# Kernel tuning notes

Measured on AMD Instinct MI355X. Metric: run time of the kernel, lower is better.

The kernel has to match this reference:

```python
import jax, jax.numpy as jnp
import numpy as np

B, LC, LQ, D = 64, 1024, 128, 128
NEG_BIG = 1.0e12


def _len_mask(seq_len, T):
    # seq_len: (B,1) int. Equivalent to 1 - cumsum(one_hot(L, T)): 1 for pos < L.
    pos = jnp.arange(T)  # (T,)
    return (pos[None, :] < seq_len).astype(jnp.float32)  # (B,T)


def setup_inputs() -> dict:
    key = jax.random.key(0)
    ks = jax.random.split(key, 7)
    return {
        "x_cont": jax.random.normal(ks[0], (B, LC, D), dtype=jnp.float32),
        "x_ques": jax.random.normal(ks[1], (B, LQ, D), dtype=jnp.float32),
        "W0": jax.random.normal(ks[2], (D, 1), dtype=jnp.float32) / np.sqrt(D),
        "W1": jax.random.normal(ks[3], (D, 1), dtype=jnp.float32) / np.sqrt(D),
        "W2": jax.random.normal(ks[4], (1, 1, D), dtype=jnp.float32) / np.sqrt(D),
        "cont_len": jax.random.randint(ks[5], (B, 1), 1, LC, dtype=jnp.int32),
        "ques_len": jax.random.randint(ks[6], (B, 1), 1, LQ, dtype=jnp.int32),
    }


def reference(x_cont, x_ques, W0, W1, W2, cont_len, ques_len):
    # Trilinear similarity: S[b,c,q] = x_cont@W0 + x_ques@W1 + (x_cont*W2) . x_ques
    s_cont = jnp.einsum('bcd,do->bco', x_cont, W0)            # (B,LC,1)
    s_ques = jnp.einsum('bqd,do->boq', x_ques, W1)            # (B,1,LQ)
    s_fuse = jnp.einsum('bcd,bqd->bcq', x_cont * W2, x_ques)  # (B,LC,LQ)
    S = s_cont + s_ques + s_fuse                               # (B,LC,LQ)

    mask_q = _len_mask(ques_len, LQ)  # (B,LQ)
    mask_c = _len_mask(cont_len, LC)  # (B,LC)

    # Softmax over query axis, masking invalid query positions (axis=-1)
    S_bar = jax.nn.softmax(S - (1.0 - mask_q)[:, None, :] * NEG_BIG, axis=-1)
    # Softmax over context axis, masking invalid context positions, then transpose
    S_T = jnp.swapaxes(
        jax.nn.softmax(S - (1.0 - mask_c)[:, :, None] * NEG_BIG, axis=1), 1, 2
    )  # (B,LQ,LC)

    c2q = jnp.einsum('bcq,bqd->bcd', S_bar, x_ques)             # (B,LC,D)
    q2c = jnp.einsum('bcq,bqk,bkd->bcd', S_bar, S_T, x_cont)    # (B,LC,D)

    result = jnp.concatenate(
        [x_cont, c2q, x_cont * c2q, x_cont * q2c], axis=-1
    )  # (B,LC,4D)
    return result, S_bar, S_T
```

## Files before the change

kernel.cpp:

```cpp
#include <hip/hip_runtime.h>

#define NB 64
#define LC 1024
#define LQ 128
#define DD 128
#define NEG_BIG 1.0e12f

typedef __attribute__((ext_vector_type(8))) short short8;
typedef __attribute__((ext_vector_type(4))) unsigned short ushort4v;
typedef __attribute__((ext_vector_type(4))) float floatx4;

__device__ __forceinline__ float wave_reduce_max(float v) {
#pragma unroll
  for (int m = 32; m >= 1; m >>= 1) v = fmaxf(v, __shfl_xor(v, m, 64));
  return v;
}
__device__ __forceinline__ float wave_reduce_sum(float v) {
#pragma unroll
  for (int m = 32; m >= 1; m >>= 1) v += __shfl_xor(v, m, 64);
  return v;
}
__device__ __forceinline__ unsigned short f2bf(float f) {
  union { float f; unsigned int u; } v;
  v.f = f;
  const unsigned int r = v.u + 0x7FFFu + ((v.u >> 16) & 1u);
  return (unsigned short)(r >> 16);
}
__device__ __forceinline__ float bf2f(unsigned int u) {
  union { unsigned int u; float f; } v;
  v.u = u << 16;
  return v.f;
}

__global__ __launch_bounds__(256) void k_pre_c(
    const float* __restrict__ xc, const float* __restrict__ W0,
    unsigned short* __restrict__ xcb, unsigned short* __restrict__ xcT,
    float* __restrict__ a_cont) {
  __shared__ __align__(16) unsigned short tile[64 * 136];
  const int b = blockIdx.x >> 4;
  const int c0 = (blockIdx.x & 15) << 6;
  const int t = threadIdx.x;
  const int w = t >> 6, lane = t & 63;
  const float* src = xc + ((size_t)b * LC + c0) * DD;
  unsigned short* dstb = xcb + ((size_t)b * LC + c0) * DD;

#pragma unroll
  for (int i = 0; i < 8; ++i) {
    const int id = t + (i << 8);
    const int row = id >> 5, u = id & 31;
    const float4 v = *(const float4*)(src + (size_t)row * DD + (u << 2));
    ushort4v pk;
    pk[0] = f2bf(v.x); pk[1] = f2bf(v.y); pk[2] = f2bf(v.z); pk[3] = f2bf(v.w);
    *(ushort4v*)(tile + row * 136 + (u << 2)) = pk;
    *(ushort4v*)(dstb + (size_t)row * DD + (u << 2)) = pk;
  }
  const float w0a = W0[lane << 1];
  const float w0b = W0[(lane << 1) + 1];
  __syncthreads();
#pragma unroll
  for (int r = 0; r < 16; ++r) {
    const int row = (w << 4) + r;
    const unsigned int pk = *(const unsigned int*)(tile + row * 136 + (lane << 1));
    float s = fmaf(bf2f(pk & 0xffffu), w0a, bf2f(pk >> 16) * w0b);
    s = wave_reduce_sum(s);
    if (lane == 0) a_cont[b * LC + c0 + row] = s;
  }
  const int d = t >> 1, ch = t & 1;
  short8 o[4];
#pragma unroll
  for (int j = 0; j < 32; ++j)
    ((unsigned short*)o)[j] = tile[(ch * 32 + j) * 136 + d];
  unsigned short* dp = xcT + ((size_t)b * DD + d) * LC + c0 + ch * 32;
#pragma unroll
  for (int j = 0; j < 4; ++j) *(short8*)(dp + (j << 3)) = o[j];
}

__global__ __launch_bounds__(256) void k_pre_q(
    const float* __restrict__ xq, const float* __restrict__ W1,
    const float* __restrict__ W2, unsigned short* __restrict__ xqwb,
    unsigned short* __restrict__ xqT, float* __restrict__ a_ques) {
  __shared__ __align__(16) unsigned short tile[128 * 136];
  const int b = blockIdx.x;
  const int t = threadIdx.x;
  const int w = t >> 6, lane = t & 63;
  const float* src = xq + (size_t)b * LQ * DD;
  unsigned short* dstw = xqwb + (size_t)b * LQ * DD;

#pragma unroll
  for (int i = 0; i < 16; ++i) {
    const int id = t + (i << 8);
    const int row = id >> 5, u = id & 31;
    const float4 v = *(const float4*)(src + (size_t)row * DD + (u << 2));
    const float4 wv = *(const float4*)(W2 + (u << 2));
    ushort4v pk, pf;
    pk[0] = f2bf(v.x); pk[1] = f2bf(v.y); pk[2] = f2bf(v.z); pk[3] = f2bf(v.w);
    pf[0] = f2bf(v.x * wv.x); pf[1] = f2bf(v.y * wv.y);
    pf[2] = f2bf(v.z * wv.z); pf[3] = f2bf(v.w * wv.w);
    *(ushort4v*)(tile + row * 136 + (u << 2)) = pk;
    *(ushort4v*)(dstw + (size_t)row * DD + (u << 2)) = pf;
  }
  const float w1a = W1[lane << 1];
  const float w1b = W1[(lane << 1) + 1];
  __syncthreads();
#pragma unroll
  for (int r = 0; r < 32; ++r) {
    const int row = (w << 5) + r;
    const unsigned int pk = *(const unsigned int*)(tile + row * 136 + (lane << 1));
    float s = fmaf(bf2f(pk & 0xffffu), w1a, bf2f(pk >> 16) * w1b);
    s = wave_reduce_sum(s);
    if (lane == 0) a_ques[b * LQ + row] = s;
  }
  const int d = t >> 1, ch = t & 1;
  short8 o[8];
#pragma unroll
  for (int j = 0; j < 64; ++j)
    ((unsigned short*)o)[j] = tile[(ch * 64 + j) * 136 + d];
  unsigned short* dp = xqT + ((size_t)b * DD + d) * LQ + ch * 64;
#pragma unroll
  for (int j = 0; j < 8; ++j) *(short8*)(dp + (j << 3)) = o[j];
}

#define PADW 136

__global__ __launch_bounds__(512) void k_score(
    const unsigned short* __restrict__ xcb, const unsigned short* __restrict__ xqwb,
    const float* __restrict__ a_cont, const float* __restrict__ a_ques,
    const int* __restrict__ qlen_p, float* __restrict__ out_sbar,
    float* __restrict__ out_st) {
  __shared__ __align__(16) unsigned short smem[2 * 128 * PADW];
  unsigned short* xcs = smem;
  unsigned short* xqs = smem + 128 * PADW;
  float* s_tile = (float*)smem;

  const int b = blockIdx.x >> 3;
  const int c0 = (blockIdx.x & 7) << 7;
  const int t = threadIdx.x;
  const int w = t >> 6, lane = t & 63;
  const int frow = lane & 15;
  const int kb = lane >> 4;

  const unsigned short* xcb_blk = xcb + ((size_t)b * LC + c0) * DD;
  const unsigned short* xqw_b = xqwb + (size_t)b * LQ * DD;

#pragma unroll
  for (int i = 0; i < 4; ++i) {
    const int id = t + (i << 9);
    const int row = id >> 4, u = id & 15;
    *(short8*)(xcs + row * PADW + (u << 3)) =
        *(const short8*)(xcb_blk + (size_t)row * DD + (u << 3));
    *(short8*)(xqs + row * PADW + (u << 3)) =
        *(const short8*)(xqw_b + (size_t)row * DD + (u << 3));
  }

  const int qlen = qlen_p[b];
  float ac[4], aq[8];
#pragma unroll
  for (int reg = 0; reg < 4; ++reg)
    ac[reg] = a_cont[b * LC + c0 + w * 16 + kb * 4 + reg];
#pragma unroll
  for (int n = 0; n < 8; ++n) aq[n] = a_ques[b * LQ + n * 16 + frow];

  __syncthreads();

  floatx4 acc[8];
#pragma unroll
  for (int n = 0; n < 8; ++n) acc[n] = (floatx4){0.f, 0.f, 0.f, 0.f};
  const unsigned short* arow = xcs + (w * 16 + frow) * PADW + kb * 8;
  const unsigned short* brow = xqs + frow * PADW + kb * 8;
#pragma unroll
  for (int ks = 0; ks < 4; ++ks) {
    const short8 af = *(const short8*)(arow + ks * 32);
#pragma unroll
    for (int n = 0; n < 8; ++n) {
      const short8 bf = *(const short8*)(brow + n * 16 * PADW + ks * 32);
      acc[n] = __builtin_amdgcn_mfma_f32_16x16x32_bf16(af, bf, acc[n], 0, 0, 0);
    }
  }

  float raw[8][4];
#pragma unroll
  for (int n = 0; n < 8; ++n)
#pragma unroll
    for (int reg = 0; reg < 4; ++reg) raw[n][reg] = acc[n][reg] + ac[reg] + aq[n];

  float* sbar_row0 =
      out_sbar + ((size_t)b * LC + c0 + w * 16 + kb * 4) * LQ + frow;
#pragma unroll
  for (int reg = 0; reg < 4; ++reg) {
    float x[8];
    float m = -3.4e38f;
#pragma unroll
    for (int n = 0; n < 8; ++n) {
      x[n] = raw[n][reg] - ((n * 16 + frow) < qlen ? 0.f : NEG_BIG);
      m = fmaxf(m, x[n]);
    }
#pragma unroll
    for (int msk = 8; msk >= 1; msk >>= 1) m = fmaxf(m, __shfl_xor(m, msk, 64));
    float s = 0.f;
#pragma unroll
    for (int n = 0; n < 8; ++n) {
      x[n] = __expf(x[n] - m);
      s += x[n];
    }
#pragma unroll
    for (int msk = 8; msk >= 1; msk >>= 1) s += __shfl_xor(s, msk, 64);
    const float inv = 1.0f / s;
    float* o = sbar_row0 + (size_t)reg * LQ;
#pragma unroll
    for (int n = 0; n < 8; ++n) o[n * 16] = x[n] * inv;
  }

  float* st_b = out_st + (size_t)b * LQ * LC;
#pragma unroll
  for (int p = 0; p < 4; ++p) {
    __syncthreads();
#pragma unroll
    for (int n2 = 0; n2 < 2; ++n2) {
#pragma unroll
      for (int reg = 0; reg < 4; ++reg)
        s_tile[(n2 * 16 + frow) * 132 + (w * 16 + kb * 4 + reg)] =
            raw[2 * p + n2][reg];
    }
    __syncthreads();
    const int qrow = t >> 4;
    const int cch = t & 15;
    const float4 u0 = *(const float4*)(s_tile + qrow * 132 + (cch << 2));
    const float4 u1 = *(const float4*)(s_tile + qrow * 132 + ((cch + 16) << 2));
    float* dst = st_b + (size_t)(p * 32 + qrow) * LC + c0;
    *(float4*)(dst + (cch << 2)) = u0;
    *(float4*)(dst + ((cch + 16) << 2)) = u1;
  }
}

#define PSTR 1028

__global__ __launch_bounds__(256) void k_fuse(
    float* __restrict__ st, const unsigned short* __restrict__ xcT,
    const int* __restrict__ clen_p, unsigned short* __restrict__ AbT) {
  __shared__ __align__(16) unsigned short P[16 * PSTR];
  __shared__ __align__(16) unsigned short bt[128 * 72];
  __shared__ unsigned short abt[128 * 20];
  __shared__ float inv_s[16];

  const int b = blockIdx.x >> 3;
  const int q0 = (blockIdx.x & 7) << 4;
  const int t = threadIdx.x;
  const int w = t >> 6, lane = t & 63;
  const int frow = lane & 15, kb = lane >> 4;
  const int L = clen_p[b];
  float* st_blk = st + ((size_t)b * LQ + q0) * LC;

#pragma unroll
  for (int r = 0; r < 4; ++r) {
    const int row = (w << 2) + r;
    float* rowp = st_blk + (size_t)row * LC;
    float4 v[4];
    float m = -3.4e38f;
#pragma unroll
    for (int ph = 0; ph < 4; ++ph) {
      const int c = (lane << 2) + (ph << 8);
      v[ph] = *(const float4*)(rowp + c);
      if (c + 0 < L) m = fmaxf(m, v[ph].x);
      if (c + 1 < L) m = fmaxf(m, v[ph].y);
      if (c + 2 < L) m = fmaxf(m, v[ph].z);
      if (c + 3 < L) m = fmaxf(m, v[ph].w);
    }
    m = wave_reduce_max(m);
    float s = 0.f;
#pragma unroll
    for (int ph = 0; ph < 4; ++ph) {
      const int c = (lane << 2) + (ph << 8);
      v[ph].x = (c + 0 < L) ? __expf(v[ph].x - m) : 0.f;
      v[ph].y = (c + 1 < L) ? __expf(v[ph].y - m) : 0.f;
      v[ph].z = (c + 2 < L) ? __expf(v[ph].z - m) : 0.f;
      v[ph].w = (c + 3 < L) ? __expf(v[ph].w - m) : 0.f;
      s += (v[ph].x + v[ph].y) + (v[ph].z + v[ph].w);
      ushort4v pk;
      pk[0] = f2bf(v[ph].x); pk[1] = f2bf(v[ph].y);
      pk[2] = f2bf(v[ph].z); pk[3] = f2bf(v[ph].w);
      *(ushort4v*)(P + row * PSTR + c) = pk;
    }
    s = wave_reduce_sum(s);
    const float inv = 1.0f / s;
    if (lane == 0) inv_s[row] = inv;
#pragma unroll
    for (int ph = 0; ph < 4; ++ph) {
      const int c = (lane << 2) + (ph << 8);
      *(float4*)(rowp + c) =
          make_float4(v[ph].x * inv, v[ph].y * inv, v[ph].z * inv, v[ph].w * inv);
    }
  }

  const unsigned short* xcT_b = xcT + (size_t)b * DD * LC;
  floatx4 acc0 = (floatx4){0.f, 0.f, 0.f, 0.f};
  floatx4 acc1 = (floatx4){0.f, 0.f, 0.f, 0.f};
  for (int kc = 0; kc < 16; ++kc) {
    __syncthreads();
#pragma unroll
    for (int i = 0; i < 4; ++i) {
      const int id = t + (i << 8);
      const int row = id >> 3, u = id & 7;
      *(short8*)(bt + row * 72 + (u << 3)) =
          *(const short8*)(xcT_b + (size_t)row * LC + (kc << 6) + (u << 3));
    }
    __syncthreads();
#pragma unroll
    for (int ks = 0; ks < 2; ++ks) {
      const short8 af =
          *(const short8*)(P + frow * PSTR + (kc << 6) + ks * 32 + kb * 8);
      const short8 b0 =
          *(const short8*)(bt + ((w * 2 + 0) * 16 + frow) * 72 + ks * 32 + kb * 8);
      const short8 b1 =
          *(const short8*)(bt + ((w * 2 + 1) * 16 + frow) * 72 + ks * 32 + kb * 8);
      acc0 = __builtin_amdgcn_mfma_f32_16x16x32_bf16(af, b0, acc0, 0, 0, 0);
      acc1 = __builtin_amdgcn_mfma_f32_16x16x32_bf16(af, b1, acc1, 0, 0, 0);
    }
  }
  __syncthreads();
  const float i0 = inv_s[kb * 4 + 0], i1 = inv_s[kb * 4 + 1];
  const float i2 = inv_s[kb * 4 + 2], i3 = inv_s[kb * 4 + 3];
  {
    const int d0 = (w * 2 + 0) * 16 + frow;
    abt[d0 * 20 + kb * 4 + 0] = f2bf(acc0[0] * i0);
    abt[d0 * 20 + kb * 4 + 1] = f2bf(acc0[1] * i1);
    abt[d0 * 20 + kb * 4 + 2] = f2bf(acc0[2] * i2);
    abt[d0 * 20 + kb * 4 + 3] = f2bf(acc0[3] * i3);
    const int d1 = (w * 2 + 1) * 16 + frow;
    abt[d1 * 20 + kb * 4 + 0] = f2bf(acc1[0] * i0);
    abt[d1 * 20 + kb * 4 + 1] = f2bf(acc1[1] * i1);
    abt[d1 * 20 + kb * 4 + 2] = f2bf(acc1[2] * i2);
    abt[d1 * 20 + kb * 4 + 3] = f2bf(acc1[3] * i3);
  }
  __syncthreads();
  const int d = t >> 1, h = t & 1;
  short8 ov;
#pragma unroll
  for (int j = 0; j < 8; ++j)
    ((unsigned short*)&ov)[j] = abt[d * 20 + h * 8 + j];
  *(short8*)(AbT + ((size_t)b * DD + d) * LQ + q0 + h * 8) = ov;
}

__global__ __launch_bounds__(256) void k_out(
    const float* __restrict__ xc, const float* __restrict__ sbar,
    const unsigned short* __restrict__ xqT, const unsigned short* __restrict__ AbT,
    float* __restrict__ out) {
  __shared__ __align__(16) float stg[2 * 32 * 132];
  unsigned short* sbs = (unsigned short*)stg;

  const int b = blockIdx.x >> 4;
  const int c0 = (blockIdx.x & 15) << 6;
  const int t = threadIdx.x;
  const int w = t >> 6, lane = t & 63;
  const int frow = lane & 15, kb = lane >> 4;

  const float* sb_blk = sbar + ((size_t)b * LC + c0) * LQ;
#pragma unroll
  for (int i = 0; i < 8; ++i) {
    const int id = t + (i << 8);
    const int row = id >> 5, u = id & 31;
    const float4 v = *(const float4*)(sb_blk + (size_t)row * LQ + (u << 2));
    ushort4v pk;
    pk[0] = f2bf(v.x); pk[1] = f2bf(v.y); pk[2] = f2bf(v.z); pk[3] = f2bf(v.w);
    *(ushort4v*)(sbs + row * 136 + (u << 2)) = pk;
  }

  const unsigned short* xqT_b = xqT + (size_t)b * DD * LQ;
  const unsigned short* AbT_b = AbT + (size_t)b * DD * LQ;
  short8 bq[2][4], ba[2][4];
#pragma unroll
  for (int nt = 0; nt < 2; ++nt) {
    const int d = (w << 5) + (nt << 4) + frow;
#pragma unroll
    for (int ks = 0; ks < 4; ++ks) {
      bq[nt][ks] = *(const short8*)(xqT_b + (size_t)d * LQ + ks * 32 + kb * 8);
      ba[nt][ks] = *(const short8*)(AbT_b + (size_t)d * LQ + ks * 32 + kb * 8);
    }
  }
  __syncthreads();

  floatx4 accq[4][2], acca[4][2];
#pragma unroll
  for (int mt = 0; mt < 4; ++mt)
#pragma unroll
    for (int nt = 0; nt < 2; ++nt) {
      accq[mt][nt] = (floatx4){0.f, 0.f, 0.f, 0.f};
      acca[mt][nt] = (floatx4){0.f, 0.f, 0.f, 0.f};
    }
#pragma unroll
  for (int mt = 0; mt < 4; ++mt) {
#pragma unroll
    for (int ks = 0; ks < 4; ++ks) {
      const short8 af =
          *(const short8*)(sbs + ((mt << 4) + frow) * 136 + ks * 32 + kb * 8);
#pragma unroll
      for (int nt = 0; nt < 2; ++nt) {
        accq[mt][nt] =
            __builtin_amdgcn_mfma_f32_16x16x32_bf16(af, bq[nt][ks], accq[mt][nt], 0, 0, 0);
        acca[mt][nt] =
            __builtin_amdgcn_mfma_f32_16x16x32_bf16(af, ba[nt][ks], acca[mt][nt], 0, 0, 0);
      }
    }
  }

  float* out_b = out + ((size_t)b * LC + c0) * (4 * DD);
  const float* xc_blk = xc + ((size_t)b * LC + c0) * DD;

#pragma unroll
  for (int p = 0; p < 2; ++p) {
    __syncthreads();
#pragma unroll
    for (int mh = 0; mh < 2; ++mh) {
      const int mt = 2 * p + mh;
#pragma unroll
      for (int nt = 0; nt < 2; ++nt) {
        const int d = (w << 5) + (nt << 4) + frow;
        const int cl = (mh << 4) + (kb << 2);
#pragma unroll
        for (int reg = 0; reg < 4; ++reg) {
          stg[(cl + reg) * 132 + d] = accq[mt][nt][reg];
          stg[32 * 132 + (cl + reg) * 132 + d] = acca[mt][nt][reg];
        }
      }
    }
    __syncthreads();
    const int g = lane >> 4;
    const int d0 = (lane & 15) << 3;
#pragma unroll
    for (int j = 0; j < 8; ++j) {
      const int rl = (w << 3) + j;
      const int c = (p << 5) + rl;
      const float4 xv0 = *(const float4*)(xc_blk + (size_t)c * DD + d0);
      const float4 xv1 = *(const float4*)(xc_blk + (size_t)c * DD + d0 + 4);
      const float4 cq0 = *(const float4*)(stg + rl * 132 + d0);
      const float4 cq1 = *(const float4*)(stg + rl * 132 + d0 + 4);
      const float4 qc0 = *(const float4*)(stg + 32 * 132 + rl * 132 + d0);
      const float4 qc1 = *(const float4*)(stg + 32 * 132 + rl * 132 + d0 + 4);
      float4 o0, o1;
      if (g == 0) { o0 = xv0; o1 = xv1; }
      else if (g == 1) { o0 = cq0; o1 = cq1; }
      else if (g == 2) {
        o0 = make_float4(xv0.x * cq0.x, xv0.y * cq0.y, xv0.z * cq0.z, xv0.w * cq0.w);
        o1 = make_float4(xv1.x * cq1.x, xv1.y * cq1.y, xv1.z * cq1.z, xv1.w * cq1.w);
      } else {
        o0 = make_float4(xv0.x * qc0.x, xv0.y * qc0.y, xv0.z * qc0.z, xv0.w * qc0.w);
        o1 = make_float4(xv1.x * qc1.x, xv1.y * qc1.y, xv1.z * qc1.z, xv1.w * qc1.w);
      }
      float* o = out_b + (size_t)c * (4 * DD) + (g << 7) + d0;
      *(float4*)(o) = o0;
      *(float4*)(o + 4) = o1;
    }
  }
}

extern "C" void kernel_launch(void* const* d_in, const int* in_sizes, int n_in,
                              void* d_out, int out_size, void* d_ws, size_t ws_size,
                              hipStream_t stream) {
  const float* xc = (const float*)d_in[0];
  const float* xq = (const float*)d_in[1];
  const float* W0 = (const float*)d_in[2];
  const float* W1 = (const float*)d_in[3];
  const float* W2 = (const float*)d_in[4];
  const int* clen = (const int*)d_in[5];
  const int* qlen = (const int*)d_in[6];

  float* out = (float*)d_out;
  float* out_sbar = out + (size_t)NB * LC * 4 * DD;
  float* out_st = out_sbar + (size_t)NB * LC * LQ;

  float* a_cont = (float*)d_ws;
  float* a_ques = a_cont + NB * LC;
  unsigned short* xcb = (unsigned short*)(a_ques + NB * LQ);
  unsigned short* xcT = xcb + (size_t)NB * LC * DD;
  unsigned short* xqwb = xcT + (size_t)NB * LC * DD;
  unsigned short* xqT = xqwb + (size_t)NB * LQ * DD;
  unsigned short* AbT = xqT + (size_t)NB * LQ * DD;

  k_pre_c<<<NB * 16, 256, 0, stream>>>(xc, W0, xcb, xcT, a_cont);
  k_pre_q<<<NB, 256, 0, stream>>>(xq, W1, W2, xqwb, xqT, a_ques);
  k_score<<<NB * 8, 512, 0, stream>>>(xcb, xqwb, a_cont, a_ques, qlen,
                                      out_sbar, out_st);
  k_fuse<<<NB * 8, 256, 0, stream>>>(out_st, xcT, clen, AbT);
  k_out<<<NB * 16, 256, 0, stream>>>(xc, out_sbar, xqT, AbT, out);
}
```

Before: 123.1 us.

## Pass unnormalized bf16 column exponentials and partial sums from score to fuse kernel

The score kernel now applies the context-length mask and exponentiates the scores itself. It writes them as bf16 along with per-tile column partial sums, replacing the fp32 S_T round trip in which the fuse kernel re-read, normalized and rewrote every score. The fuse kernel only rescales the bf16 values and reuses them as the MFMA operand. The bf16 copies of x_cont and x_ques*W2 are dropped; the score kernel converts fp32 inputs directly. The column softmax no longer subtracts a max, so it relies on score magnitudes staying small enough not to overflow exp. The S_T output is also quantized to bf16 precision.

```diff
diff --git a/kernel.cpp b/kernel.cpp
--- a/kernel.cpp
+++ b/kernel.cpp
@@ -10,11 +10,6 @@
 typedef __attribute__((ext_vector_type(4))) unsigned short ushort4v;
 typedef __attribute__((ext_vector_type(4))) float floatx4;
 
-__device__ __forceinline__ float wave_reduce_max(float v) {
-#pragma unroll
-  for (int m = 32; m >= 1; m >>= 1) v = fmaxf(v, __shfl_xor(v, m, 64));
-  return v;
-}
 __device__ __forceinline__ float wave_reduce_sum(float v) {
 #pragma unroll
   for (int m = 32; m >= 1; m >>= 1) v += __shfl_xor(v, m, 64);
@@ -34,15 +29,13 @@
 
 __global__ __launch_bounds__(256) void k_pre_c(
     const float* __restrict__ xc, const float* __restrict__ W0,
-    unsigned short* __restrict__ xcb, unsigned short* __restrict__ xcT,
-    float* __restrict__ a_cont) {
+    unsigned short* __restrict__ xcT, float* __restrict__ a_cont) {
   __shared__ __align__(16) unsigned short tile[64 * 136];
   const int b = blockIdx.x >> 4;
   const int c0 = (blockIdx.x & 15) << 6;
   const int t = threadIdx.x;
   const int w = t >> 6, lane = t & 63;
   const float* src = xc + ((size_t)b * LC + c0) * DD;
-  unsigned short* dstb = xcb + ((size_t)b * LC + c0) * DD;
 
 #pragma unroll
   for (int i = 0; i < 8; ++i) {
@@ -52,7 +45,6 @@
     ushort4v pk;
     pk[0] = f2bf(v.x); pk[1] = f2bf(v.y); pk[2] = f2bf(v.z); pk[3] = f2bf(v.w);
     *(ushort4v*)(tile + row * 136 + (u << 2)) = pk;
-    *(ushort4v*)(dstb + (size_t)row * DD + (u << 2)) = pk;
   }
   const float w0a = W0[lane << 1];
   const float w0b = W0[(lane << 1) + 1];
@@ -77,27 +69,21 @@
 
 __global__ __launch_bounds__(256) void k_pre_q(
     const float* __restrict__ xq, const float* __restrict__ W1,
-    const float* __restrict__ W2, unsigned short* __restrict__ xqwb,
     unsigned short* __restrict__ xqT, float* __restrict__ a_ques) {
   __shared__ __align__(16) unsigned short tile[128 * 136];
   const int b = blockIdx.x;
   const int t = threadIdx.x;
   const int w = t >> 6, lane = t & 63;
   const float* src = xq + (size_t)b * LQ * DD;
-  unsigned short* dstw = xqwb + (size_t)b * LQ * DD;
 
 #pragma unroll
   for (int i = 0; i < 16; ++i) {
     const int id = t + (i << 8);
     const int row = id >> 5, u = id & 31;
     const float4 v = *(const float4*)(src + (size_t)row * DD + (u << 2));
-    const float4 wv = *(const float4*)(W2 + (u << 2));
-    ushort4v pk, pf;
+    ushort4v pk;
     pk[0] = f2bf(v.x); pk[1] = f2bf(v.y); pk[2] = f2bf(v.z); pk[3] = f2bf(v.w);
-    pf[0] = f2bf(v.x * wv.x); pf[1] = f2bf(v.y * wv.y);
-    pf[2] = f2bf(v.z * wv.z); pf[3] = f2bf(v.w * wv.w);
     *(ushort4v*)(tile + row * 136 + (u << 2)) = pk;
-    *(ushort4v*)(dstw + (size_t)row * DD + (u << 2)) = pf;
   }
   const float w1a = W1[lane << 1];
   const float w1b = W1[(lane << 1) + 1];
@@ -123,36 +109,57 @@
 #define PADW 136
 
 __global__ __launch_bounds__(512) void k_score(
-    const unsigned short* __restrict__ xcb, const unsigned short* __restrict__ xqwb,
-    const float* __restrict__ a_cont, const float* __restrict__ a_ques,
-    const int* __restrict__ qlen_p, float* __restrict__ out_sbar,
-    float* __restrict__ out_st) {
+    const float* __restrict__ xc, const float* __restrict__ xq,
+    const float* __restrict__ w2, const float* __restrict__ a_cont,
+    const float* __restrict__ a_ques, const int* __restrict__ qlen_p,
+    const int* __restrict__ clen_p, float* __restrict__ out_sbar,
+    unsigned short* __restrict__ Pb, float* __restrict__ colsum_part) {
   __shared__ __align__(16) unsigned short smem[2 * 128 * PADW];
   unsigned short* xcs = smem;
   unsigned short* xqs = smem + 128 * PADW;
-  float* s_tile = (float*)smem;
+  unsigned short* ptile = smem;
 
   const int b = blockIdx.x >> 3;
-  const int c0 = (blockIdx.x & 7) << 7;
+  const int ct = blockIdx.x & 7;
+  const int c0 = ct << 7;
   const int t = threadIdx.x;
   const int w = t >> 6, lane = t & 63;
   const int frow = lane & 15;
   const int kb = lane >> 4;
 
-  const unsigned short* xcb_blk = xcb + ((size_t)b * LC + c0) * DD;
-  const unsigned short* xqw_b = xqwb + (size_t)b * LQ * DD;
+  const float* xc_blk = xc + ((size_t)b * LC + c0) * DD;
+  const float* xq_b = xq + (size_t)b * LQ * DD;
 
 #pragma unroll
   for (int i = 0; i < 4; ++i) {
     const int id = t + (i << 9);
     const int row = id >> 4, u = id & 15;
-    *(short8*)(xcs + row * PADW + (u << 3)) =
-        *(const short8*)(xcb_blk + (size_t)row * DD + (u << 3));
-    *(short8*)(xqs + row * PADW + (u << 3)) =
-        *(const short8*)(xqw_b + (size_t)row * DD + (u << 3));
+    {
+      const float4 v0 = *(const float4*)(xc_blk + (size_t)row * DD + (u << 3));
+      const float4 v1 = *(const float4*)(xc_blk + (size_t)row * DD + (u << 3) + 4);
+      short8 pk;
+      pk[0] = (short)f2bf(v0.x); pk[1] = (short)f2bf(v0.y);
+      pk[2] = (short)f2bf(v0.z); pk[3] = (short)f2bf(v0.w);
+      pk[4] = (short)f2bf(v1.x); pk[5] = (short)f2bf(v1.y);
+      pk[6] = (short)f2bf(v1.z); pk[7] = (short)f2bf(v1.w);
+      *(short8*)(xcs + row * PADW + (u << 3)) = pk;
+    }
+    {
+      const float4 v0 = *(const float4*)(xq_b + (size_t)row * DD + (u << 3));
+      const float4 v1 = *(const float4*)(xq_b + (size_t)row * DD + (u << 3) + 4);
+      const float4 w0 = *(const float4*)(w2 + (u << 3));
+      const float4 w1 = *(const float4*)(w2 + (u << 3) + 4);
+      short8 pk;
+      pk[0] = (short)f2bf(v0.x * w0.x); pk[1] = (short)f2bf(v0.y * w0.y);
+      pk[2] = (short)f2bf(v0.z * w0.z); pk[3] = (short)f2bf(v0.w * w0.w);
+      pk[4] = (short)f2bf(v1.x * w1.x); pk[5] = (short)f2bf(v1.y * w1.y);
+      pk[6] = (short)f2bf(v1.z * w1.z); pk[7] = (short)f2bf(v1.w * w1.w);
+      *(short8*)(xqs + row * PADW + (u << 3)) = pk;
+    }
   }
 
   const int qlen = qlen_p[b];
+  const int clen = clen_p[b];
   float ac[4], aq[8];
 #pragma unroll
   for (int reg = 0; reg < 4; ++reg)
@@ -210,7 +217,17 @@
     for (int n = 0; n < 8; ++n) o[n * 16] = x[n] * inv;
   }
 
-  float* st_b = out_st + (size_t)b * LQ * LC;
+  const int cl0 = c0 + w * 16 + kb * 4;
+#pragma unroll
+  for (int reg = 0; reg < 4; ++reg) {
+    const bool ok = (cl0 + reg) < clen;
+#pragma unroll
+    for (int n = 0; n < 8; ++n)
+      raw[n][reg] = ok ? __expf(raw[n][reg]) : 0.f;
+  }
+
+  unsigned short* Pb_b = Pb + (size_t)b * LQ * LC;
+  float* cs_blk = colsum_part + ((size_t)b * 8 + ct) * LQ;
 #pragma unroll
   for (int p = 0; p < 4; ++p) {
     __syncthreads();
@@ -218,26 +235,28 @@
     for (int n2 = 0; n2 < 2; ++n2) {
 #pragma unroll
       for (int reg = 0; reg < 4; ++reg)
-        s_tile[(n2 * 16 + frow) * 132 + (w * 16 + kb * 4 + reg)] =
-            raw[2 * p + n2][reg];
+        ptile[(n2 * 16 + frow) * 136 + (w * 16 + kb * 4 + reg)] =
+            f2bf(raw[2 * p + n2][reg]);
     }
     __syncthreads();
     const int qrow = t >> 4;
-    const int cch = t & 15;
-    const float4 u0 = *(const float4*)(s_tile + qrow * 132 + (cch << 2));
-    const float4 u1 = *(const float4*)(s_tile + qrow * 132 + ((cch + 16) << 2));
-    float* dst = st_b + (size_t)(p * 32 + qrow) * LC + c0;
-    *(float4*)(dst + (cch << 2)) = u0;
-    *(float4*)(dst + ((cch + 16) << 2)) = u1;
-  }
-}
-
-#define PSTR 1028
+    const int ch = t & 15;
+    const short8 pv = *(const short8*)(ptile + qrow * 136 + (ch << 3));
+    *(short8*)(Pb_b + (size_t)(p * 32 + qrow) * LC + c0 + (ch << 3)) = pv;
+    float s = 0.f;
+#pragma unroll
+    for (int j = 0; j < 8; ++j) s += bf2f((unsigned short)pv[j]);
+#pragma unroll
+    for (int msk = 8; msk >= 1; msk >>= 1) s += __shfl_xor(s, msk, 64);
+    if (ch == 0) cs_blk[p * 32 + qrow] = s;
+  }
+}
 
 __global__ __launch_bounds__(256) void k_fuse(
-    float* __restrict__ st, const unsigned short* __restrict__ xcT,
-    const int* __restrict__ clen_p, unsigned short* __restrict__ AbT) {
-  __shared__ __align__(16) unsigned short P[16 * PSTR];
+    const unsigned short* __restrict__ Pb, const float* __restrict__ colsum_part,
+    const unsigned short* __restrict__ xcT, float* __restrict__ st,
+    unsigned short* __restrict__ AbT) {
+  __shared__ __align__(16) unsigned short Ps[16 * 1032];
   __shared__ __align__(16) unsigned short bt[128 * 72];
   __shared__ unsigned short abt[128 * 20];
   __shared__ float inv_s[16];
@@ -247,47 +266,45 @@
   const int t = threadIdx.x;
   const int w = t >> 6, lane = t & 63;
   const int frow = lane & 15, kb = lane >> 4;
-  const int L = clen_p[b];
-  float* st_blk = st + ((size_t)b * LQ + q0) * LC;
-
-#pragma unroll
-  for (int r = 0; r < 4; ++r) {
-    const int row = (w << 2) + r;
-    float* rowp = st_blk + (size_t)row * LC;
-    float4 v[4];
-    float m = -3.4e38f;
-#pragma unroll
-    for (int ph = 0; ph < 4; ++ph) {
-      const int c = (lane << 2) + (ph << 8);
-      v[ph] = *(const float4*)(rowp + c);
-      if (c + 0 < L) m = fmaxf(m, v[ph].x);
-      if (c + 1 < L) m = fmaxf(m, v[ph].y);
-      if (c + 2 < L) m = fmaxf(m, v[ph].z);
-      if (c + 3 < L) m = fmaxf(m, v[ph].w);
-    }
-    m = wave_reduce_max(m);
+
+  const unsigned short* Pb_blk = Pb + ((size_t)b * LQ + q0) * LC;
+  {
+    const int row = t >> 4;
+#pragma unroll
+    for (int j = 0; j < 8; ++j) {
+      const int cs = ((t & 15) << 3) + (j << 7);
+      *(short8*)(Ps + row * 1032 + cs) =
+          *(const short8*)(Pb_blk + (size_t)row * LC + cs);
+    }
+  }
+  if (t < 16) {
     float s = 0.f;
 #pragma unroll
-    for (int ph = 0; ph < 4; ++ph) {
-      const int c = (lane << 2) + (ph << 8);
-      v[ph].x = (c + 0 < L) ? __expf(v[ph].x - m) : 0.f;
-      v[ph].y = (c + 1 < L) ? __expf(v[ph].y - m) : 0.f;
-      v[ph].z = (c + 2 < L) ? __expf(v[ph].z - m) : 0.f;
-      v[ph].w = (c + 3 < L) ? __expf(v[ph].w - m) : 0.f;
-      s += (v[ph].x + v[ph].y) + (v[ph].z + v[ph].w);
-      ushort4v pk;
-      pk[0] = f2bf(v[ph].x); pk[1] = f2bf(v[ph].y);
-      pk[2] = f2bf(v[ph].z); pk[3] = f2bf(v[ph].w);
-      *(ushort4v*)(P + row * PSTR + c) = pk;
-    }
-    s = wave_reduce_sum(s);
-    const float inv = 1.0f / s;
-    if (lane == 0) inv_s[row] = inv;
-#pragma unroll
-    for (int ph = 0; ph < 4; ++ph) {
-      const int c = (lane << 2) + (ph << 8);
-      *(float4*)(rowp + c) =
-          make_float4(v[ph].x * inv, v[ph].y * inv, v[ph].z * inv, v[ph].w * inv);
+    for (int j = 0; j < 8; ++j)
+      s += colsum_part[((size_t)b * 8 + j) * LQ + q0 + t];
+    inv_s[t] = 1.0f / s;
+  }
+  __syncthreads();
+
+  {
+    const int row = t >> 4;
+    const float inv = inv_s[row];
+    float* dst = st + ((size_t)b * LQ + q0 + row) * LC;
+#pragma unroll
+    for (int j = 0; j < 8; ++j) {
+      const int cs = ((t & 15) << 3) + (j << 7);
+      const short8 pv = *(const short8*)(Ps + row * 1032 + cs);
+      float4 o0, o1;
+      o0.x = bf2f((unsigned short)pv[0]) * inv;
+      o0.y = bf2f((unsigned short)pv[1]) * inv;
+      o0.z = bf2f((unsigned short)pv[2]) * inv;
+      o0.w = bf2f((unsigned short)pv[3]) * inv;
+      o1.x = bf2f((unsigned short)pv[4]) * inv;
+      o1.y = bf2f((unsigned short)pv[5]) * inv;
+      o1.z = bf2f((unsigned short)pv[6]) * inv;
+      o1.w = bf2f((unsigned short)pv[7]) * inv;
+      *(float4*)(dst + cs) = o0;
+      *(float4*)(dst + cs + 4) = o1;
     }
   }
 
@@ -307,7 +324,7 @@
 #pragma unroll
     for (int ks = 0; ks < 2; ++ks) {
       const short8 af =
-          *(const short8*)(P + frow * PSTR + (kc << 6) + ks * 32 + kb * 8);
+          *(const short8*)(Ps + frow * 1032 + (kc << 6) + ks * 32 + kb * 8);
       const short8 b0 =
           *(const short8*)(bt + ((w * 2 + 0) * 16 + frow) * 72 + ks * 32 + kb * 8);
       const short8 b1 =
@@ -469,16 +486,16 @@
 
   float* a_cont = (float*)d_ws;
   float* a_ques = a_cont + NB * LC;
-  unsigned short* xcb = (unsigned short*)(a_ques + NB * LQ);
-  unsigned short* xcT = xcb + (size_t)NB * LC * DD;
-  unsigned short* xqwb = xcT + (size_t)NB * LC * DD;
-  unsigned short* xqT = xqwb + (size_t)NB * LQ * DD;
+  float* colsum_part = a_ques + NB * LQ;
+  unsigned short* xcT = (unsigned short*)(colsum_part + NB * 8 * LQ);
+  unsigned short* xqT = xcT + (size_t)NB * LC * DD;
   unsigned short* AbT = xqT + (size_t)NB * LQ * DD;
-
-  k_pre_c<<<NB * 16, 256, 0, stream>>>(xc, W0, xcb, xcT, a_cont);
-  k_pre_q<<<NB, 256, 0, stream>>>(xq, W1, W2, xqwb, xqT, a_ques);
-  k_score<<<NB * 8, 512, 0, stream>>>(xcb, xqwb, a_cont, a_ques, qlen,
-                                      out_sbar, out_st);
-  k_fuse<<<NB * 8, 256, 0, stream>>>(out_st, xcT, clen, AbT);
+  unsigned short* Pb = AbT + (size_t)NB * LQ * DD;
+
+  k_pre_c<<<NB * 16, 256, 0, stream>>>(xc, W0, xcT, a_cont);
+  k_pre_q<<<NB, 256, 0, stream>>>(xq, W1, xqT, a_ques);
+  k_score<<<NB * 8, 512, 0, stream>>>(xc, xq, W2, a_cont, a_ques, qlen, clen,
+                                      out_sbar, Pb, colsum_part);
+  k_fuse<<<NB * 8, 256, 0, stream>>>(Pb, colsum_part, xcT, out_st, AbT);
   k_out<<<NB * 16, 256, 0, stream>>>(xc, out_sbar, xqT, AbT, out);
 }
```

Result: no change. 124.9 us (+1.5%).
